# Kernel optimization log

Hardware: AMD Instinct MI355X
Metric: run time of the kernel (lower is better)

## Reference

```python
import jax, jax.numpy as jnp
import numpy as np

N, E = 30000, 480000
IN_C, HID, HEADS = 128, 32, 8
HC = HID * HEADS  # 256
EPS = 1e-5
NEG_SLOPE = 0.2


def setup_inputs() -> dict:
    key = jax.random.key(0)
    ks = jax.random.split(key, 20)
    s = 0.05
    return {
        "x": jax.random.normal(ks[0], (N, IN_C), jnp.float32),
        "edge_index": jax.random.randint(ks[1], (2, E), 0, N, jnp.int32),
        "W1": jax.random.normal(ks[2], (IN_C, HC), jnp.float32) * s,
        "a1_src": jax.random.normal(ks[3], (HEADS, HID), jnp.float32) * s,
        "a1_dst": jax.random.normal(ks[4], (HEADS, HID), jnp.float32) * s,
        "b1": jnp.zeros((HC,), jnp.float32),
        "g1": jnp.ones((HC,), jnp.float32),
        "be1": jnp.zeros((HC,), jnp.float32),
        "W2": jax.random.normal(ks[5], (HC, HC), jnp.float32) * s,
        "a2_src": jax.random.normal(ks[6], (HEADS, HID), jnp.float32) * s,
        "a2_dst": jax.random.normal(ks[7], (HEADS, HID), jnp.float32) * s,
        "b2": jnp.zeros((HC,), jnp.float32),
        "g2": jnp.ones((HC,), jnp.float32),
        "be2": jnp.zeros((HC,), jnp.float32),
        "lW1": jax.random.normal(ks[8], (HC, HID), jnp.float32) * s,
        "lb1": jnp.zeros((HID,), jnp.float32),
        "lW2": jax.random.normal(ks[9], (HID, 1), jnp.float32) * s,
        "lb2": jnp.zeros((1,), jnp.float32),
    }


def gat_layer(x, src, dst, W, a_s, a_d, b):
    # x: [N, Fin] -> h: [N, H, C]
    h = (x @ W).reshape(N, HEADS, HID)
    al_s = jnp.sum(h * a_s, axis=-1)  # [N, H]
    al_d = jnp.sum(h * a_d, axis=-1)  # [N, H]
    e = jax.nn.leaky_relu(al_s[src] + al_d[dst], NEG_SLOPE)  # [E', H]
    # segment softmax over incoming edges of each destination node
    e = e - jax.ops.segment_max(e, dst, num_segments=N)[dst]
    ex = jnp.exp(e)
    alpha = ex / jax.ops.segment_sum(ex, dst, num_segments=N)[dst]
    msg = h[src] * alpha[:, :, None]  # [E', H, C]
    out = jax.ops.segment_sum(msg, dst, num_segments=N)  # [N, H, C]
    return out.reshape(N, HC) + b


def batchnorm(x, g, b):
    m = jnp.mean(x, axis=0)
    v = jnp.var(x, axis=0)
    return (x - m) * jax.lax.rsqrt(v + EPS) * g + b


def reference(x, edge_index, W1, a1_src, a1_dst, b1, g1, be1,
              W2, a2_src, a2_dst, b2, g2, be2, lW1, lb1, lW2, lb2):
    # add self-loops (PyG GATConv default)
    loop = jnp.arange(N, dtype=edge_index.dtype)
    src = jnp.concatenate([edge_index[0], loop])
    dst = jnp.concatenate([edge_index[1], loop])

    h = jax.nn.elu(gat_layer(x, src, dst, W1, a1_src, a1_dst, b1))
    h = batchnorm(h, g1, be1)
    h = jax.nn.elu(gat_layer(h, src, dst, W2, a2_src, a2_dst, b2))
    h = batchnorm(h, g2, be2)
    h = jax.nn.elu(h @ lW1 + lb1)
    return h @ lW2 + lb2
```

## Files before the change

### kernel.cpp

```cpp
#include <hip/hip_runtime.h>
#include <math.h>

#define N_NODES 30000
#define E_EDGES 480000
#define EP (E_EDGES + N_NODES)
#define IN_CH 128
#define HID 32
#define HEADS 8
#define HC 256
#define BN_EPS 1e-5f
#define NEG_SLOPE 0.2f
#define SCAN_NB ((N_NODES + 1023) / 1024)
#define PART_SLOTS 64
#define M_PAD 30080

typedef __attribute__((ext_vector_type(8))) short bf16x8;
typedef __attribute__((ext_vector_type(4))) float f32x4;

__device__ __forceinline__ float elu_f(float x) { return x > 0.f ? x : __expf(x) - 1.f; }
__device__ __forceinline__ float lrelu_f(float x) { return x >= 0.f ? x : NEG_SLOPE * x; }
__device__ __forceinline__ float bf2f(unsigned short u) {
    return __uint_as_float(((unsigned)u) << 16);
}
__device__ __forceinline__ unsigned short f2bf(float f) {
    unsigned u = __float_as_uint(f);
    return (unsigned short)((u + 0x7fffu + ((u >> 16) & 1u)) >> 16);
}

#define GLD16(gp, lp)                                                      \
    __builtin_amdgcn_global_load_lds(                                      \
        (const __attribute__((address_space(1))) unsigned int*)(gp),       \
        (__attribute__((address_space(3))) unsigned int*)(lp), 16, 0, 0)

__global__ void wt_all_kernel(const float* __restrict__ W1,
                              unsigned short* __restrict__ wt1) {
    int i = blockIdx.x * 256 + threadIdx.x;
    if (i < IN_CH * HC) {
        int k = i >> 8, n = i & 255;
        wt1[(size_t)n * IN_CH + k] = f2bf(W1[i]);
    }
}

__global__ void xconv_kernel(const float* __restrict__ x, unsigned short* __restrict__ xbf) {
    int i = blockIdx.x * 256 + threadIdx.x;
    if (i * 8 >= N_NODES * IN_CH) return;
    const float4* xp = (const float4*)(x + (size_t)i * 8);
    float4 v0 = xp[0], v1 = xp[1];
    ushort4 o0, o1;
    o0.x = f2bf(v0.x); o0.y = f2bf(v0.y); o0.z = f2bf(v0.z); o0.w = f2bf(v0.w);
    o1.x = f2bf(v1.x); o1.y = f2bf(v1.y); o1.z = f2bf(v1.z); o1.w = f2bf(v1.w);
    ushort4* op = (ushort4*)(xbf + (size_t)i * 8);
    op[0] = o0; op[1] = o1;
}

__global__ __launch_bounds__(256) void fold2_kernel(const float* __restrict__ W2,
                                                    const float* __restrict__ part,
                                                    const float* __restrict__ g,
                                                    const float* __restrict__ be,
                                                    unsigned short* __restrict__ wt2p,
                                                    float* __restrict__ cb2) {
    __shared__ float red[256];
    int n = blockIdx.x, k = threadIdx.x;
    float s = 0.f, qq = 0.f;
#pragma unroll
    for (int b = 0; b < PART_SLOTS; ++b) {
        s += part[(size_t)b * 512 + k];
        qq += part[(size_t)b * 512 + 256 + k];
    }
    float mn = s / (float)N_NODES;
    float var = qq / (float)N_NODES - mn * mn;
    float istd = rsqrtf(var + BN_EPS);
    float sck = istd * g[k];
    float shk = be[k] - mn * sck;
    float w = W2[(size_t)k * HC + n];
    wt2p[(size_t)n * HC + k] = f2bf(w * sck);
    red[k] = shk * w;
    __syncthreads();
    for (int off = 128; off > 0; off >>= 1) {
        if (k < off) red[k] += red[k + off];
        __syncthreads();
    }
    if (k == 0) cb2[n] = red[0];
}

__global__ __launch_bounds__(256) void fold3_kernel(const float* __restrict__ lW1,
                                                    const float* __restrict__ part,
                                                    const float* __restrict__ g,
                                                    const float* __restrict__ be,
                                                    const float* __restrict__ lb1,
                                                    unsigned short* __restrict__ wtmp,
                                                    float* __restrict__ lb1p) {
    __shared__ float red[256];
    int n = blockIdx.x, k = threadIdx.x;
    float s = 0.f, qq = 0.f;
#pragma unroll
    for (int b = 0; b < PART_SLOTS; ++b) {
        s += part[(size_t)b * 512 + k];
        qq += part[(size_t)b * 512 + 256 + k];
    }
    float mn = s / (float)N_NODES;
    float var = qq / (float)N_NODES - mn * mn;
    float istd = rsqrtf(var + BN_EPS);
    float sck = istd * g[k];
    float shk = be[k] - mn * sck;
    float w = lW1[(size_t)k * HID + n];
    wtmp[(size_t)n * HC + k] = f2bf(w * sck);
    red[k] = shk * w;
    __syncthreads();
    for (int off = 128; off > 0; off >>= 1) {
        if (k < off) red[k] += red[k + off];
        __syncthreads();
    }
    if (k == 0) lb1p[n] = lb1[n] + red[0];
}

__global__ __launch_bounds__(512) void gemm_mfma(const unsigned short* __restrict__ Abf,
                                                 const unsigned short* __restrict__ Bt,
                                                 const float* __restrict__ cb,
                                                 unsigned short* __restrict__ C,
                                                 float* __restrict__ al_s,
                                                 float* __restrict__ al_d,
                                                 const float* __restrict__ a_src,
                                                 const float* __restrict__ a_dst,
                                                 int M, int K) {
    __shared__ __align__(16) unsigned short As[128 * 32];
    __shared__ __align__(16) unsigned short Bs[256 * 32];
    int tid = threadIdx.x;
    int wave = tid >> 6, lane = tid & 63;
    int m = lane & 15, q = lane >> 4;
    int wr = (wave >> 2) * 64;
    int hp = wave & 3;
    int col0 = hp * 64;
    int row0 = blockIdx.x * 128;

    int sA = wave * 64 + lane;
    int rA = sA >> 2, scA = sA & 3;
    int ccA = scA ^ (rA & 3) ^ ((rA >> 2) & 3);
    const unsigned short* aSrc = Abf + (size_t)(row0 + rA) * K + ccA * 8;
    unsigned short* aDst = As + wave * 512;
    int sB0 = wave * 128 + lane;
    int rB0 = sB0 >> 2, scB0 = sB0 & 3;
    int ccB0 = scB0 ^ (rB0 & 3) ^ ((rB0 >> 2) & 3);
    const unsigned short* bSrc0 = Bt + (size_t)rB0 * K + ccB0 * 8;
    unsigned short* bDst0 = Bs + wave * 1024;
    int sB1 = sB0 + 64;
    int rB1 = sB1 >> 2, scB1 = sB1 & 3;
    int ccB1 = scB1 ^ (rB1 & 3) ^ ((rB1 >> 2) & 3);
    const unsigned short* bSrc1 = Bt + (size_t)rB1 * K + ccB1 * 8;
    unsigned short* bDst1 = Bs + wave * 1024 + 512;

    int ccr8 = (q ^ (m & 3) ^ ((m >> 2) & 3)) * 8;

    f32x4 acc[4][4];
#pragma unroll
    for (int i = 0; i < 4; ++i)
#pragma unroll
        for (int j = 0; j < 4; ++j) acc[i][j] = (f32x4){0.f, 0.f, 0.f, 0.f};

    for (int k0 = 0; k0 < K; k0 += 32) {
        GLD16(aSrc + k0, aDst);
        GLD16(bSrc0 + k0, bDst0);
        GLD16(bSrc1 + k0, bDst1);
        __syncthreads();
        bf16x8 a0 = *(const bf16x8*)(As + (wr + m) * 32 + ccr8);
        bf16x8 a1 = *(const bf16x8*)(As + (wr + 16 + m) * 32 + ccr8);
        bf16x8 a2 = *(const bf16x8*)(As + (wr + 32 + m) * 32 + ccr8);
        bf16x8 a3 = *(const bf16x8*)(As + (wr + 48 + m) * 32 + ccr8);
#pragma unroll
        for (int ni = 0; ni < 4; ++ni) {
            bf16x8 b = *(const bf16x8*)(Bs + (col0 + ni * 16 + m) * 32 + ccr8);
            acc[0][ni] = __builtin_amdgcn_mfma_f32_16x16x32_bf16(a0, b, acc[0][ni], 0, 0, 0);
            acc[1][ni] = __builtin_amdgcn_mfma_f32_16x16x32_bf16(a1, b, acc[1][ni], 0, 0, 0);
            acc[2][ni] = __builtin_amdgcn_mfma_f32_16x16x32_bf16(a2, b, acc[2][ni], 0, 0, 0);
            acc[3][ni] = __builtin_amdgcn_mfma_f32_16x16x32_bf16(a3, b, acc[3][ni], 0, 0, 0);
        }
        __syncthreads();
    }
    float cbv[4];
#pragma unroll
    for (int ni = 0; ni < 4; ++ni) cbv[ni] = cb[col0 + ni * 16 + m];
#pragma unroll
    for (int mi = 0; mi < 4; ++mi)
#pragma unroll
        for (int ni = 0; ni < 4; ++ni)
#pragma unroll
            for (int r = 0; r < 4; ++r) acc[mi][ni][r] += cbv[ni];

    float asv[4], adv[4];
#pragma unroll
    for (int ni = 0; ni < 4; ++ni) {
        asv[ni] = a_src[col0 + ni * 16 + m];
        adv[ni] = a_dst[col0 + ni * 16 + m];
    }
#pragma unroll
    for (int mi = 0; mi < 4; ++mi) {
#pragma unroll
        for (int r = 0; r < 4; ++r) {
            int grow = row0 + wr + mi * 16 + q * 4 + r;
            bool gv = grow < M;
            if (gv) {
#pragma unroll
                for (int ni = 0; ni < 4; ++ni)
                    C[(size_t)grow * HC + col0 + ni * 16 + m] = f2bf(acc[mi][ni][r]);
            }
            float ps0 = acc[mi][0][r] * asv[0] + acc[mi][1][r] * asv[1];
            float pd0 = acc[mi][0][r] * adv[0] + acc[mi][1][r] * adv[1];
            float ps1 = acc[mi][2][r] * asv[2] + acc[mi][3][r] * asv[3];
            float pd1 = acc[mi][2][r] * adv[2] + acc[mi][3][r] * adv[3];
            ps0 += __shfl_xor(ps0, 1); pd0 += __shfl_xor(pd0, 1);
            ps1 += __shfl_xor(ps1, 1); pd1 += __shfl_xor(pd1, 1);
            ps0 += __shfl_xor(ps0, 2); pd0 += __shfl_xor(pd0, 2);
            ps1 += __shfl_xor(ps1, 2); pd1 += __shfl_xor(pd1, 2);
            ps0 += __shfl_xor(ps0, 4); pd0 += __shfl_xor(pd0, 4);
            ps1 += __shfl_xor(ps1, 4); pd1 += __shfl_xor(pd1, 4);
            ps0 += __shfl_xor(ps0, 8); pd0 += __shfl_xor(pd0, 8);
            ps1 += __shfl_xor(ps1, 8); pd1 += __shfl_xor(pd1, 8);
            if (gv) {
                if (m == 0) {
                    al_s[grow * HEADS + 2 * hp] = ps0;
                    al_d[grow * HEADS + 2 * hp] = pd0;
                } else if (m == 1) {
                    al_s[grow * HEADS + 2 * hp + 1] = ps1;
                    al_d[grow * HEADS + 2 * hp + 1] = pd1;
                }
            }
        }
    }
}

__global__ void deg_kernel(const int* __restrict__ ei, int* __restrict__ deg,
                           float* __restrict__ part) {
    int e = blockIdx.x * blockDim.x + threadIdx.x;
    if (e < 2 * PART_SLOTS * 512 + 256) part[e] = 0.f;
    if (e >= EP) return;
    int d = (e < E_EDGES) ? ei[E_EDGES + e] : e - E_EDGES;
    atomicAdd(deg + d, 1);
}

__global__ __launch_bounds__(1024) void scan_blk(const int* __restrict__ deg,
                                                 int* __restrict__ rs,
                                                 int* __restrict__ bsum) {
    __shared__ int sh[1024];
    int t = threadIdx.x;
    int i = blockIdx.x * 1024 + t;
    int v = (i < N_NODES) ? deg[i] : 0;
    sh[t] = v;
    __syncthreads();
    for (int off = 1; off < 1024; off <<= 1) {
        int tv = (t >= off) ? sh[t - off] : 0;
        __syncthreads();
        sh[t] += tv;
        __syncthreads();
    }
    if (i < N_NODES) rs[i] = sh[t] - v;
    if (t == 1023) bsum[blockIdx.x] = sh[1023];
}

__global__ __launch_bounds__(1024) void scan_add(int* __restrict__ rs,
                                                 int* __restrict__ cursor,
                                                 const int* __restrict__ bsum) {
    __shared__ int sh_off, sh_tot;
    int t = threadIdx.x;
    if (t < 64) {
        int v = (t < SCAN_NB) ? bsum[t] : 0;
        int pre = (t < (int)blockIdx.x) ? v : 0;
        int tot = v;
#pragma unroll
        for (int off = 1; off < 64; off <<= 1) {
            tot += __shfl_xor(tot, off);
            pre += __shfl_xor(pre, off);
        }
        if (t == 0) { sh_off = pre; sh_tot = tot; }
    }
    __syncthreads();
    int i = blockIdx.x * 1024 + t;
    if (i < N_NODES) {
        int v = rs[i] + sh_off;
        rs[i] = v;
        cursor[i] = v;
    } else if (i == N_NODES) {
        rs[N_NODES] = sh_tot;
    }
}

__global__ void scatter_kernel(const int* __restrict__ ei, int* __restrict__ cursor,
                               int* __restrict__ csr_src) {
    int e = blockIdx.x * blockDim.x + threadIdx.x;
    if (e >= EP) return;
    int s, d;
    if (e < E_EDGES) { s = ei[e]; d = ei[E_EDGES + e]; } else { s = d = e - E_EDGES; }
    int pos = atomicAdd(cursor + d, 1);
    csr_src[pos] = s;
}

__global__ __launch_bounds__(256) void attn_kernel(const uint4* __restrict__ h8,
                                                   const float* __restrict__ al_s,
                                                   const float* __restrict__ al_d,
                                                   const int* __restrict__ row_start,
                                                   const int* __restrict__ csr_src,
                                                   const float4* __restrict__ bias4,
                                                   uint4* __restrict__ out8,
                                                   float* __restrict__ part) {
    __shared__ float lds_s[4][256];
    __shared__ float lds_q[4][256];
    int wave = threadIdx.x >> 6;
    int d = blockIdx.x * 4 + wave;
    int lane = threadIdx.x & 63;
    int hh = lane & 7, eo = lane >> 3;
    int g = lane >> 5, c = lane & 31;
    int hl = c >> 2;
    int beg = row_start[d], end = row_start[d + 1];
    float ad = al_d[d * HEADS + hh];
    float ssum = 0.f;
    float acc[8];
#pragma unroll
    for (int t = 0; t < 8; ++t) acc[t] = 0.f;

#define PAIR_BODY(p)                                                      \
    {                                                                     \
        int e0 = 2 * (p) + g;                                             \
        int sj = __shfl(sreg, e0 * 8);                                    \
        float aj = __shfl(ex, e0 * 8 + hl);                               \
        uint4 v = h8[(size_t)sj * 32 + c];                                \
        acc[0] += aj * bf2f((unsigned short)v.x);                         \
        acc[1] += aj * bf2f((unsigned short)(v.x >> 16));                 \
        acc[2] += aj * bf2f((unsigned short)v.y);                         \
        acc[3] += aj * bf2f((unsigned short)(v.y >> 16));                 \
        acc[4] += aj * bf2f((unsigned short)v.z);                         \
        acc[5] += aj * bf2f((unsigned short)(v.z >> 16));                 \
        acc[6] += aj * bf2f((unsigned short)v.w);                         \
        acc[7] += aj * bf2f((unsigned short)(v.w >> 16));                 \
    }

    for (int i = beg; i < end; i += 8) {
        int chunk = end - i;
        if (chunk > 8) chunk = 8;
        int sreg = 0;
        float ex = 0.f;
        if (eo < chunk) {
            sreg = csr_src[i + eo];
            ex = __expf(lrelu_f(al_s[sreg * HEADS + hh] + ad));
        }
        ssum += ex;
        if (chunk == 8) {
#pragma unroll
            for (int p = 0; p < 4; ++p) PAIR_BODY(p);
        } else {
            int np = (chunk + 1) >> 1;
            for (int p = 0; p < np; ++p) PAIR_BODY(p);
        }
    }
#undef PAIR_BODY

#pragma unroll
    for (int t = 0; t < 8; ++t) acc[t] += __shfl_xor(acc[t], 32);
    ssum += __shfl_xor(ssum, 8);
    ssum += __shfl_xor(ssum, 16);
    ssum += __shfl_xor(ssum, 32);
    float inv = 1.f / __shfl(ssum, hl);

    float4 b0 = bias4[c * 2], b1 = bias4[c * 2 + 1];
    float o0 = elu_f(acc[0] * inv + b0.x);
    float o1 = elu_f(acc[1] * inv + b0.y);
    float o2 = elu_f(acc[2] * inv + b0.z);
    float o3 = elu_f(acc[3] * inv + b0.w);
    float o4 = elu_f(acc[4] * inv + b1.x);
    float o5 = elu_f(acc[5] * inv + b1.y);
    float o6 = elu_f(acc[6] * inv + b1.z);
    float o7 = elu_f(acc[7] * inv + b1.w);

    if (g == 0) {
        uint4 ov;
        ov.x = (unsigned)f2bf(o0) | ((unsigned)f2bf(o1) << 16);
        ov.y = (unsigned)f2bf(o2) | ((unsigned)f2bf(o3) << 16);
        ov.z = (unsigned)f2bf(o4) | ((unsigned)f2bf(o5) << 16);
        ov.w = (unsigned)f2bf(o6) | ((unsigned)f2bf(o7) << 16);
        out8[(size_t)d * 32 + c] = ov;
        int cb = c * 8;
        lds_s[wave][cb + 0] = o0; lds_q[wave][cb + 0] = o0 * o0;
        lds_s[wave][cb + 1] = o1; lds_q[wave][cb + 1] = o1 * o1;
        lds_s[wave][cb + 2] = o2; lds_q[wave][cb + 2] = o2 * o2;
        lds_s[wave][cb + 3] = o3; lds_q[wave][cb + 3] = o3 * o3;
        lds_s[wave][cb + 4] = o4; lds_q[wave][cb + 4] = o4 * o4;
        lds_s[wave][cb + 5] = o5; lds_q[wave][cb + 5] = o5 * o5;
        lds_s[wave][cb + 6] = o6; lds_q[wave][cb + 6] = o6 * o6;
        lds_s[wave][cb + 7] = o7; lds_q[wave][cb + 7] = o7 * o7;
    }
    __syncthreads();
    int ch = threadIdx.x;
    float s = lds_s[0][ch] + lds_s[1][ch] + lds_s[2][ch] + lds_s[3][ch];
    float q = lds_q[0][ch] + lds_q[1][ch] + lds_q[2][ch] + lds_q[3][ch];
    float* pb = part + (size_t)(blockIdx.x & (PART_SLOTS - 1)) * 512;
    atomicAdd(pb + ch, s);
    atomicAdd(pb + 256 + ch, q);
}

__global__ __launch_bounds__(256) void mlp_mfma(const unsigned short* __restrict__ in,
                                                const unsigned short* __restrict__ Wt,
                                                const float* __restrict__ lb1p,
                                                const float* __restrict__ lW2,
                                                const float* __restrict__ lb2,
                                                float* __restrict__ out) {
    int tid = threadIdx.x;
    int wave = tid >> 6, lane = tid & 63;
    int m = lane & 15, q = lane >> 4;
    int rbase = blockIdx.x * 64 + wave * 16;
    int arow = rbase + m;
    bool valid = arow < N_NODES;
    const unsigned short* ap = in + (size_t)arow * HC;
    f32x4 acc0 = (f32x4){0.f, 0.f, 0.f, 0.f}, acc1 = acc0;
#pragma unroll
    for (int k0 = 0; k0 < HC; k0 += 32) {
        int c0 = k0 + q * 8;
        bf16x8 b0 = *(const bf16x8*)(Wt + (size_t)m * HC + c0);
        bf16x8 b1 = *(const bf16x8*)(Wt + (size_t)(m + 16) * HC + c0);
        bf16x8 a = (bf16x8){0, 0, 0, 0, 0, 0, 0, 0};
        if (valid) a = *(const bf16x8*)(ap + c0);
        acc0 = __builtin_amdgcn_mfma_f32_16x16x32_bf16(a, b0, acc0, 0, 0, 0);
        acc1 = __builtin_amdgcn_mfma_f32_16x16x32_bf16(a, b1, acc1, 0, 0, 0);
    }
    float w2a = lW2[m], w2b = lW2[m + 16];
    float ba = lb1p[m], bb = lb1p[m + 16];
#pragma unroll
    for (int r = 0; r < 4; ++r) {
        float v = elu_f(acc0[r] + ba) * w2a + elu_f(acc1[r] + bb) * w2b;
        v += __shfl_xor(v, 1);
        v += __shfl_xor(v, 2);
        v += __shfl_xor(v, 4);
        v += __shfl_xor(v, 8);
        int orow = rbase + q * 4 + r;
        if (m == 0 && orow < N_NODES) out[orow] = v + lb2[0];
    }
}

extern "C" void kernel_launch(void* const* d_in, const int* in_sizes, int n_in,
                              void* d_out, int out_size, void* d_ws, size_t ws_size,
                              hipStream_t stream) {
    const float* x   = (const float*)d_in[0];
    const int*   ei  = (const int*)d_in[1];
    const float* W1  = (const float*)d_in[2];
    const float* a1s = (const float*)d_in[3];
    const float* a1d = (const float*)d_in[4];
    const float* b1  = (const float*)d_in[5];
    const float* g1  = (const float*)d_in[6];
    const float* be1 = (const float*)d_in[7];
    const float* W2  = (const float*)d_in[8];
    const float* a2s = (const float*)d_in[9];
    const float* a2d = (const float*)d_in[10];
    const float* b2  = (const float*)d_in[11];
    const float* g2  = (const float*)d_in[12];
    const float* be2 = (const float*)d_in[13];
    const float* lW1 = (const float*)d_in[14];
    const float* lb1 = (const float*)d_in[15];
    const float* lW2 = (const float*)d_in[16];
    const float* lb2 = (const float*)d_in[17];
    float* out = (float*)d_out;

    char* p = (char*)d_ws;
    auto alloc = [&](size_t bytes) {
        char* r = p;
        p += (bytes + 255) & ~(size_t)255;
        return r;
    };
    unsigned short* x_bf  = (unsigned short*)alloc((size_t)M_PAD * IN_CH * 2);
    unsigned short* h_bf  = (unsigned short*)alloc((size_t)N_NODES * HC * 2);
    unsigned short* o_bf  = (unsigned short*)alloc((size_t)M_PAD * HC * 2);
    unsigned short* wt1   = (unsigned short*)alloc((size_t)IN_CH * HC * 2);
    unsigned short* wt2p  = (unsigned short*)alloc((size_t)HC * HC * 2);
    unsigned short* wtmp  = (unsigned short*)alloc((size_t)HC * HID * 2);
    float* f_als  = (float*)alloc((size_t)N_NODES * HEADS * 4);
    float* f_ald  = (float*)alloc((size_t)N_NODES * HEADS * 4);
    int*   i_deg  = (int*)alloc((size_t)N_NODES * 4);
    int*   i_rs   = (int*)alloc((size_t)(N_NODES + 1) * 4);
    int*   i_cur  = (int*)alloc((size_t)N_NODES * 4);
    int*   i_src  = (int*)alloc((size_t)EP * 4);
    int*   i_bsum = (int*)alloc((size_t)(SCAN_NB + 1) * 4);
    float* f_part = (float*)alloc(((size_t)2 * PART_SLOTS * 512 + 256) * 4);
    float* f_cb2  = (float*)alloc(HC * 4);
    float* f_lb1p = (float*)alloc(HID * 4);

    float* part1 = f_part;
    float* part2 = f_part + (size_t)PART_SLOTS * 512;
    float* cb0   = f_part + (size_t)2 * PART_SLOTS * 512;

    int eb = (EP + 255) / 256;

    hipMemsetAsync(i_deg, 0, (size_t)N_NODES * 4, stream);
    deg_kernel<<<eb, 256, 0, stream>>>(ei, i_deg, f_part);
    scan_blk<<<SCAN_NB, 1024, 0, stream>>>(i_deg, i_rs, i_bsum);
    scan_add<<<SCAN_NB, 1024, 0, stream>>>(i_rs, i_cur, i_bsum);
    scatter_kernel<<<eb, 256, 0, stream>>>(ei, i_cur, i_src);

    wt_all_kernel<<<(IN_CH * HC + 255) / 256, 256, 0, stream>>>(W1, wt1);
    xconv_kernel<<<(N_NODES * IN_CH / 8 + 255) / 256, 256, 0, stream>>>(x, x_bf);

    int gblocks = (N_NODES + 127) / 128;

    gemm_mfma<<<gblocks, 512, 0, stream>>>(x_bf, wt1, cb0, h_bf, f_als, f_ald, a1s, a1d,
                                           N_NODES, IN_CH);
    attn_kernel<<<N_NODES / 4, 256, 0, stream>>>((const uint4*)h_bf, f_als, f_ald,
                                                 i_rs, i_src, (const float4*)b1,
                                                 (uint4*)o_bf, part1);
    fold2_kernel<<<HC, 256, 0, stream>>>(W2, part1, g1, be1, wt2p, f_cb2);
    gemm_mfma<<<gblocks, 512, 0, stream>>>(o_bf, wt2p, f_cb2, h_bf, f_als, f_ald, a2s, a2d,
                                           N_NODES, HC);
    attn_kernel<<<N_NODES / 4, 256, 0, stream>>>((const uint4*)h_bf, f_als, f_ald,
                                                 i_rs, i_src, (const float4*)b2,
                                                 (uint4*)o_bf, part2);
    fold3_kernel<<<HID, 256, 0, stream>>>(lW1, part2, g2, be2, lb1, wtmp, f_lb1p);
    mlp_mfma<<<(N_NODES + 63) / 64, 256, 0, stream>>>(o_bf, wtmp, f_lb1p, lW2, lb2, out);
}
```

Before: 296.0 us.

## Double-buffer GEMM loads, single-block scan, merge conversions, prefetch attention edges

The GEMM now double-buffers its A/B tiles in LDS, so the global-to-LDS loads for the next K-slice are issued while MFMAs run on the current one. The two-kernel prefix scan is replaced by one 1024-thread block that scans from shared memory. The x and W1 bf16 conversion kernels are merged into one launch. The attention loop prefetches the next chunk's source indices and logits to hide gather latency. Together these cut launch count and expose memory/compute overlap, at the cost of doubled LDS use in the GEMM and a serial single-block scan.

Result: slower. 323.8 us (+9.4%).

```diff
diff --git a/kernel.cpp b/kernel.cpp
--- a/kernel.cpp
+++ b/kernel.cpp
@@ -10,9 +10,9 @@
 #define HC 256
 #define BN_EPS 1e-5f
 #define NEG_SLOPE 0.2f
-#define SCAN_NB ((N_NODES + 1023) / 1024)
 #define PART_SLOTS 64
 #define M_PAD 30080
+#define SCAN_PAD 30720
 
 typedef __attribute__((ext_vector_type(8))) short bf16x8;
 typedef __attribute__((ext_vector_type(4))) float f32x4;
@@ -32,25 +32,26 @@
         (const __attribute__((address_space(1))) unsigned int*)(gp),       \
         (__attribute__((address_space(3))) unsigned int*)(lp), 16, 0, 0)
 
-__global__ void wt_all_kernel(const float* __restrict__ W1,
-                              unsigned short* __restrict__ wt1) {
+__global__ void conv_all_kernel(const float* __restrict__ x, const float* __restrict__ W1,
+                                unsigned short* __restrict__ xbf,
+                                unsigned short* __restrict__ wt1) {
     int i = blockIdx.x * 256 + threadIdx.x;
-    if (i < IN_CH * HC) {
-        int k = i >> 8, n = i & 255;
-        wt1[(size_t)n * IN_CH + k] = f2bf(W1[i]);
-    }
-}
-
-__global__ void xconv_kernel(const float* __restrict__ x, unsigned short* __restrict__ xbf) {
-    int i = blockIdx.x * 256 + threadIdx.x;
-    if (i * 8 >= N_NODES * IN_CH) return;
-    const float4* xp = (const float4*)(x + (size_t)i * 8);
-    float4 v0 = xp[0], v1 = xp[1];
-    ushort4 o0, o1;
-    o0.x = f2bf(v0.x); o0.y = f2bf(v0.y); o0.z = f2bf(v0.z); o0.w = f2bf(v0.w);
-    o1.x = f2bf(v1.x); o1.y = f2bf(v1.y); o1.z = f2bf(v1.z); o1.w = f2bf(v1.w);
-    ushort4* op = (ushort4*)(xbf + (size_t)i * 8);
-    op[0] = o0; op[1] = o1;
+    const int XB = N_NODES * IN_CH / 8;
+    if (i < XB) {
+        const float4* xp = (const float4*)(x + (size_t)i * 8);
+        float4 v0 = xp[0], v1 = xp[1];
+        ushort4 o0, o1;
+        o0.x = f2bf(v0.x); o0.y = f2bf(v0.y); o0.z = f2bf(v0.z); o0.w = f2bf(v0.w);
+        o1.x = f2bf(v1.x); o1.y = f2bf(v1.y); o1.z = f2bf(v1.z); o1.w = f2bf(v1.w);
+        ushort4* op = (ushort4*)(xbf + (size_t)i * 8);
+        op[0] = o0; op[1] = o1;
+    } else {
+        int j = i - XB;
+        if (j < IN_CH * HC) {
+            int k = j >> 8, n = j & 255;
+            wt1[(size_t)n * IN_CH + k] = f2bf(W1[j]);
+        }
+    }
 }
 
 __global__ __launch_bounds__(256) void fold2_kernel(const float* __restrict__ W2,
@@ -123,8 +124,10 @@
                                                  const float* __restrict__ a_src,
                                                  const float* __restrict__ a_dst,
                                                  int M, int K) {
-    __shared__ __align__(16) unsigned short As[128 * 32];
-    __shared__ __align__(16) unsigned short Bs[256 * 32];
+    __shared__ __align__(16) unsigned short As0[128 * 32];
+    __shared__ __align__(16) unsigned short Bs0[256 * 32];
+    __shared__ __align__(16) unsigned short As1[128 * 32];
+    __shared__ __align__(16) unsigned short Bs1[256 * 32];
     int tid = threadIdx.x;
     int wave = tid >> 6, lane = tid & 63;
     int m = lane & 15, q = lane >> 4;
@@ -137,17 +140,21 @@
     int rA = sA >> 2, scA = sA & 3;
     int ccA = scA ^ (rA & 3) ^ ((rA >> 2) & 3);
     const unsigned short* aSrc = Abf + (size_t)(row0 + rA) * K + ccA * 8;
-    unsigned short* aDst = As + wave * 512;
     int sB0 = wave * 128 + lane;
     int rB0 = sB0 >> 2, scB0 = sB0 & 3;
     int ccB0 = scB0 ^ (rB0 & 3) ^ ((rB0 >> 2) & 3);
     const unsigned short* bSrc0 = Bt + (size_t)rB0 * K + ccB0 * 8;
-    unsigned short* bDst0 = Bs + wave * 1024;
     int sB1 = sB0 + 64;
     int rB1 = sB1 >> 2, scB1 = sB1 & 3;
     int ccB1 = scB1 ^ (rB1 & 3) ^ ((rB1 >> 2) & 3);
     const unsigned short* bSrc1 = Bt + (size_t)rB1 * K + ccB1 * 8;
-    unsigned short* bDst1 = Bs + wave * 1024 + 512;
+
+    unsigned short* aD0 = As0 + wave * 512;
+    unsigned short* bD00 = Bs0 + wave * 1024;
+    unsigned short* bD01 = Bs0 + wave * 1024 + 512;
+    unsigned short* aD1 = As1 + wave * 512;
+    unsigned short* bD10 = Bs1 + wave * 1024;
+    unsigned short* bD11 = Bs1 + wave * 1024 + 512;
 
     int ccr8 = (q ^ (m & 3) ^ ((m >> 2) & 3)) * 8;
 
@@ -157,25 +164,45 @@
 #pragma unroll
         for (int j = 0; j < 4; ++j) acc[i][j] = (f32x4){0.f, 0.f, 0.f, 0.f};
 
-    for (int k0 = 0; k0 < K; k0 += 32) {
-        GLD16(aSrc + k0, aDst);
-        GLD16(bSrc0 + k0, bDst0);
-        GLD16(bSrc1 + k0, bDst1);
-        __syncthreads();
-        bf16x8 a0 = *(const bf16x8*)(As + (wr + m) * 32 + ccr8);
-        bf16x8 a1 = *(const bf16x8*)(As + (wr + 16 + m) * 32 + ccr8);
-        bf16x8 a2 = *(const bf16x8*)(As + (wr + 32 + m) * 32 + ccr8);
-        bf16x8 a3 = *(const bf16x8*)(As + (wr + 48 + m) * 32 + ccr8);
-#pragma unroll
-        for (int ni = 0; ni < 4; ++ni) {
-            bf16x8 b = *(const bf16x8*)(Bs + (col0 + ni * 16 + m) * 32 + ccr8);
-            acc[0][ni] = __builtin_amdgcn_mfma_f32_16x16x32_bf16(a0, b, acc[0][ni], 0, 0, 0);
-            acc[1][ni] = __builtin_amdgcn_mfma_f32_16x16x32_bf16(a1, b, acc[1][ni], 0, 0, 0);
-            acc[2][ni] = __builtin_amdgcn_mfma_f32_16x16x32_bf16(a2, b, acc[2][ni], 0, 0, 0);
-            acc[3][ni] = __builtin_amdgcn_mfma_f32_16x16x32_bf16(a3, b, acc[3][ni], 0, 0, 0);
-        }
-        __syncthreads();
-    }
+#define STAGE0(kk) { GLD16(aSrc + (kk), aD0); GLD16(bSrc0 + (kk), bD00); GLD16(bSrc1 + (kk), bD01); }
+#define STAGE1(kk) { GLD16(aSrc + (kk), aD1); GLD16(bSrc0 + (kk), bD10); GLD16(bSrc1 + (kk), bD11); }
+#define COMPUTE(AS, BS)                                                              \
+    {                                                                                \
+        bf16x8 a0 = *(const bf16x8*)((AS) + (wr + m) * 32 + ccr8);                   \
+        bf16x8 a1 = *(const bf16x8*)((AS) + (wr + 16 + m) * 32 + ccr8);              \
+        bf16x8 a2 = *(const bf16x8*)((AS) + (wr + 32 + m) * 32 + ccr8);              \
+        bf16x8 a3 = *(const bf16x8*)((AS) + (wr + 48 + m) * 32 + ccr8);              \
+        _Pragma("unroll")                                                            \
+        for (int ni = 0; ni < 4; ++ni) {                                             \
+            bf16x8 b = *(const bf16x8*)((BS) + (col0 + ni * 16 + m) * 32 + ccr8);    \
+            acc[0][ni] = __builtin_amdgcn_mfma_f32_16x16x32_bf16(a0, b, acc[0][ni], 0, 0, 0); \
+            acc[1][ni] = __builtin_amdgcn_mfma_f32_16x16x32_bf16(a1, b, acc[1][ni], 0, 0, 0); \
+            acc[2][ni] = __builtin_amdgcn_mfma_f32_16x16x32_bf16(a2, b, acc[2][ni], 0, 0, 0); \
+            acc[3][ni] = __builtin_amdgcn_mfma_f32_16x16x32_bf16(a3, b, acc[3][ni], 0, 0, 0); \
+        }                                                                            \
+    }
+#define SYNC_TILE                                                                    \
+    {                                                                                \
+        asm volatile("s_waitcnt vmcnt(0)" ::: "memory");                             \
+        __builtin_amdgcn_s_barrier();                                                \
+        __builtin_amdgcn_sched_barrier(0);                                           \
+    }
+
+    STAGE0(0);
+    SYNC_TILE;
+    for (int k0 = 0; k0 < K; k0 += 64) {
+        STAGE1(k0 + 32);
+        COMPUTE(As0, Bs0);
+        SYNC_TILE;
+        if (k0 + 64 < K) STAGE0(k0 + 64);
+        COMPUTE(As1, Bs1);
+        if (k0 + 64 < K) SYNC_TILE;
+    }
+#undef STAGE0
+#undef STAGE1
+#undef COMPUTE
+#undef SYNC_TILE
+
     float cbv[4];
 #pragma unroll
     for (int ni = 0; ni < 4; ++ni) cbv[ni] = cb[col0 + ni * 16 + m];
@@ -237,50 +264,34 @@
     atomicAdd(deg + d, 1);
 }
 
-__global__ __launch_bounds__(1024) void scan_blk(const int* __restrict__ deg,
+__global__ __launch_bounds__(1024) void scan_all(const int* __restrict__ deg,
                                                  int* __restrict__ rs,
-                                                 int* __restrict__ bsum) {
-    __shared__ int sh[1024];
+                                                 int* __restrict__ cursor) {
+    __shared__ int sdeg[SCAN_PAD];
+    __shared__ int partial[1024];
     int t = threadIdx.x;
-    int i = blockIdx.x * 1024 + t;
-    int v = (i < N_NODES) ? deg[i] : 0;
-    sh[t] = v;
+    for (int j = t; j < SCAN_PAD; j += 1024) sdeg[j] = (j < N_NODES) ? deg[j] : 0;
+    __syncthreads();
+    int base = t * 30;
+    int s = 0;
+#pragma unroll
+    for (int j = 0; j < 30; ++j) s += sdeg[base + j];
+    partial[t] = s;
     __syncthreads();
     for (int off = 1; off < 1024; off <<= 1) {
-        int tv = (t >= off) ? sh[t - off] : 0;
+        int tv = (t >= off) ? partial[t - off] : 0;
         __syncthreads();
-        sh[t] += tv;
+        partial[t] += tv;
         __syncthreads();
     }
-    if (i < N_NODES) rs[i] = sh[t] - v;
-    if (t == 1023) bsum[blockIdx.x] = sh[1023];
-}
-
-__global__ __launch_bounds__(1024) void scan_add(int* __restrict__ rs,
-                                                 int* __restrict__ cursor,
-                                                 const int* __restrict__ bsum) {
-    __shared__ int sh_off, sh_tot;
-    int t = threadIdx.x;
-    if (t < 64) {
-        int v = (t < SCAN_NB) ? bsum[t] : 0;
-        int pre = (t < (int)blockIdx.x) ? v : 0;
-        int tot = v;
-#pragma unroll
-        for (int off = 1; off < 64; off <<= 1) {
-            tot += __shfl_xor(tot, off);
-            pre += __shfl_xor(pre, off);
-        }
-        if (t == 0) { sh_off = pre; sh_tot = tot; }
-    }
-    __syncthreads();
-    int i = blockIdx.x * 1024 + t;
-    if (i < N_NODES) {
-        int v = rs[i] + sh_off;
-        rs[i] = v;
-        cursor[i] = v;
-    } else if (i == N_NODES) {
-        rs[N_NODES] = sh_tot;
-    }
+    int run = partial[t] - s;
+#pragma unroll
+    for (int j = 0; j < 30; ++j) {
+        int i = base + j;
+        if (i < N_NODES) { rs[i] = run; cursor[i] = run; }
+        run += sdeg[base + j];
+    }
+    if (t == 1023) rs[N_NODES] = run;
 }
 
 __global__ void scatter_kernel(const int* __restrict__ ei, int* __restrict__ cursor,
@@ -332,14 +343,25 @@
         acc[7] += aj * bf2f((unsigned short)(v.w >> 16));                 \
     }
 
-    for (int i = beg; i < end; i += 8) {
-        int chunk = end - i;
-        if (chunk > 8) chunk = 8;
-        int sreg = 0;
-        float ex = 0.f;
-        if (eo < chunk) {
-            sreg = csr_src[i + eo];
-            ex = __expf(lrelu_f(al_s[sreg * HEADS + hh] + ad));
+    int i = beg;
+    int chunk = end - i;
+    if (chunk > 8) chunk = 8;
+    int sreg = 0;
+    float ex = 0.f;
+    if (eo < chunk) {
+        sreg = csr_src[i + eo];
+        ex = __expf(lrelu_f(al_s[sreg * HEADS + hh] + ad));
+    }
+    while (i < end) {
+        int inext = i + 8;
+        int cnext = end - inext;
+        if (cnext > 8) cnext = 8;
+        int sreg_n = 0;
+        float al_n = 0.f;
+        bool pn = (cnext > 0) & (eo < cnext);
+        if (pn) {
+            sreg_n = csr_src[inext + eo];
+            al_n = al_s[sreg_n * HEADS + hh];
         }
         ssum += ex;
         if (chunk == 8) {
@@ -349,6 +371,10 @@
             int np = (chunk + 1) >> 1;
             for (int p = 0; p < np; ++p) PAIR_BODY(p);
         }
+        ex = pn ? __expf(lrelu_f(al_n + ad)) : 0.f;
+        sreg = sreg_n;
+        i = inext;
+        chunk = cnext;
     }
 #undef PAIR_BODY
 
@@ -474,7 +500,6 @@
     int*   i_rs   = (int*)alloc((size_t)(N_NODES + 1) * 4);
     int*   i_cur  = (int*)alloc((size_t)N_NODES * 4);
     int*   i_src  = (int*)alloc((size_t)EP * 4);
-    int*   i_bsum = (int*)alloc((size_t)(SCAN_NB + 1) * 4);
     float* f_part = (float*)alloc(((size_t)2 * PART_SLOTS * 512 + 256) * 4);
     float* f_cb2  = (float*)alloc(HC * 4);
     float* f_lb1p = (float*)alloc(HID * 4);
@@ -487,12 +512,11 @@
 
     hipMemsetAsync(i_deg, 0, (size_t)N_NODES * 4, stream);
     deg_kernel<<<eb, 256, 0, stream>>>(ei, i_deg, f_part);
-    scan_blk<<<SCAN_NB, 1024, 0, stream>>>(i_deg, i_rs, i_bsum);
-    scan_add<<<SCAN_NB, 1024, 0, stream>>>(i_rs, i_cur, i_bsum);
+    scan_all<<<1, 1024, 0, stream>>>(i_deg, i_rs, i_cur);
     scatter_kernel<<<eb, 256, 0, stream>>>(ei, i_cur, i_src);
 
-    wt_all_kernel<<<(IN_CH * HC + 255) / 256, 256, 0, stream>>>(W1, wt1);
-    xconv_kernel<<<(N_NODES * IN_CH / 8 + 255) / 256, 256, 0, stream>>>(x, x_bf);
+    int ctot = N_NODES * IN_CH / 8 + IN_CH * HC;
+    conv_all_kernel<<<(ctot + 255) / 256, 256, 0, stream>>>(x, W1, x_bf, wt1);
 
     int gblocks = (N_NODES + 127) / 128;
 
```
